# Kernel optimization log

Measured on AMD Instinct MI355X. Metric: run time of the kernel, lower is better.

The kernel has to match this reference:

```python
import jax, jax.numpy as jnp
import numpy as np
from jax import lax

D2 = 712  # 2*(CHAR_EMBED_DIM+ELMO_EMBED_DIM)


def _char_cnn(chars, char_emb, conv_w, conv_b):
    # chars [T,L] int -> [T,100]; batched version of the per-token conv loop
    x = char_emb[chars]                      # [T,L,100]
    x = jnp.transpose(x, (0, 2, 1))          # [T,100,L]
    y = lax.conv_general_dilated(x, conv_w, (1,), [(2, 2)],
                                 dimension_numbers=('NCH', 'OIH', 'NCH'))
    y = y + conv_b[None, :, None]
    return y.max(axis=2)


def _highway(x, pw, pb, gw, gb):
    for i in range(2):
        g = jax.nn.sigmoid(x @ gw[i].T + gb[i])
        p = jax.nn.relu(x @ pw[i].T + pb[i])
        x = g * p + (1.0 - g) * x
    return x


def _lstm_scan(x, Wih, Whh, b, h0, c0):
    # x [T,in]; torch gate order i,f,g,o
    xW = x @ Wih.T + b                       # [T,4H]
    def step(carry, xt):
        h, c = carry
        z = xt + h @ Whh.T
        i, f, g, o = jnp.split(z, 4, axis=-1)
        c = jax.nn.sigmoid(f) * c + jax.nn.sigmoid(i) * jnp.tanh(g)
        h = jax.nn.sigmoid(o) * jnp.tanh(c)
        return (h, c), h
    _, hs = lax.scan(step, (h0, c0), xW)
    return hs


def _bilstm(x, Wih, Whh, b, h0):
    # h0 [2,H]; original uses same tensor for h0 and c0
    f = _lstm_scan(x, Wih[0], Whh[0], b[0], h0[0], h0[0])
    bk = _lstm_scan(x[::-1], Wih[1], Whh[1], b[1], h0[1], h0[1])[::-1]
    return jnp.concatenate([f, bk], axis=-1)


def _forward(chars_ctx, chars_qry, elmo_ctx, elmo_qry, char_emb, conv_w, conv_b,
             hw_plain_w, hw_plain_b, hw_gate_w, hw_gate_b,
             ctx_Wih, ctx_Whh, ctx_b, sim_w,
             mod1_Wih, mod1_Whh, mod1_b, mod2_Wih, mod2_Whh, mod2_b,
             pos_Wih, pos_Whh, pos_b, pos1_w, pos2_w,
             h0_ctx_c, h0_ctx_q, h0_mod, h0_pos):
    def embed(chars, elmo, h0):
        cnn = _char_cnn(chars, char_emb, conv_w, conv_b)
        x = jnp.concatenate([cnn, elmo], axis=1)           # [T,356]
        x = _highway(x, hw_plain_w, hw_plain_b, hw_gate_w, hw_gate_b)
        return _bilstm(x, ctx_Wih, ctx_Whh, ctx_b, h0)     # [T,712]

    C = embed(chars_ctx, elmo_ctx, h0_ctx_c)   # [Tc,712]
    Q = embed(chars_qry, elmo_qry, h0_ctx_q)   # [Tq,712]

    # similarity alpha([c;q;c*q]) decomposed (no bias -> exact same math)
    w_c, w_q, w_cq = sim_w[:D2], sim_w[D2:2 * D2], sim_w[2 * D2:]
    sim = (C @ w_c)[:, None] + (Q @ w_q)[None, :] + (C * w_cq) @ Q.T  # [Tc,Tq]

    c2q = jax.nn.softmax(sim, axis=1) @ Q                  # [Tc,712]
    q2c = jax.nn.softmax(sim.max(axis=1), axis=0) @ C      # [712]
    qac = jnp.concatenate([C, c2q, C * c2q, C * q2c[None, :]], axis=1)  # [Tc,2848]

    M = _bilstm(qac, mod1_Wih, mod1_Whh, mod1_b, h0_mod[0:2])
    M = _bilstm(M, mod2_Wih, mod2_Whh, mod2_b, h0_mod[2:4])  # [Tc,712]

    pos1 = jax.nn.softmax(jnp.concatenate([qac, M], axis=1) @ pos1_w, axis=0)

    M2 = _bilstm(M, pos_Wih, pos_Whh, pos_b, h0_pos)        # [Tc,712]
    pos2 = jax.nn.softmax(jnp.concatenate([qac, M2], axis=1) @ pos2_w, axis=0)
    return pos1, pos2


def setup_inputs() -> dict:
    key = jax.random.key(0)
    ks = jax.random.split(key, 32)
    s = 0.05
    d = {
        'chars_ctx': jax.random.randint(ks[0], (4096, 16), 0, 96, dtype=jnp.int32),
        'chars_qry': jax.random.randint(ks[1], (128, 16), 0, 96, dtype=jnp.int32),
        'elmo_ctx': jax.random.normal(ks[2], (4096, 256), jnp.float32),
        'elmo_qry': jax.random.normal(ks[3], (128, 256), jnp.float32),
        'char_emb': jax.random.normal(ks[4], (96, 100), jnp.float32),
        'conv_w': jax.random.normal(ks[5], (100, 100, 5), jnp.float32) * s,
        'conv_b': jnp.zeros((100,), jnp.float32),
        'hw_plain_w': jax.random.normal(ks[6], (2, 356, 356), jnp.float32) * s,
        'hw_plain_b': jnp.zeros((2, 356), jnp.float32),
        'hw_gate_w': jax.random.normal(ks[7], (2, 356, 356), jnp.float32) * s,
        'hw_gate_b': jnp.zeros((2, 356), jnp.float32),
        'ctx_Wih': jax.random.normal(ks[8], (2, 1424, 356), jnp.float32) * s,
        'ctx_Whh': jax.random.normal(ks[9], (2, 1424, 356), jnp.float32) * s,
        'ctx_b': jnp.zeros((2, 1424), jnp.float32),
        'sim_w': jax.random.normal(ks[10], (2136,), jnp.float32) * s,
        'mod1_Wih': jax.random.normal(ks[11], (2, 1424, 2848), jnp.float32) * s,
        'mod1_Whh': jax.random.normal(ks[12], (2, 1424, 356), jnp.float32) * s,
        'mod1_b': jnp.zeros((2, 1424), jnp.float32),
        'mod2_Wih': jax.random.normal(ks[13], (2, 1424, 712), jnp.float32) * s,
        'mod2_Whh': jax.random.normal(ks[14], (2, 1424, 356), jnp.float32) * s,
        'mod2_b': jnp.zeros((2, 1424), jnp.float32),
        'pos_Wih': jax.random.normal(ks[15], (2, 1424, 712), jnp.float32) * s,
        'pos_Whh': jax.random.normal(ks[16], (2, 1424, 356), jnp.float32) * s,
        'pos_b': jnp.zeros((2, 1424), jnp.float32),
        'pos1_w': jax.random.normal(ks[17], (3560,), jnp.float32) * s,
        'pos2_w': jax.random.normal(ks[18], (3560,), jnp.float32) * s,
        'h0_ctx_c': jax.random.normal(ks[19], (2, 356), jnp.float32) * 0.1,
        'h0_ctx_q': jax.random.normal(ks[20], (2, 356), jnp.float32) * 0.1,
        'h0_mod': jax.random.normal(ks[21], (4, 356), jnp.float32) * 0.1,
        'h0_pos': jax.random.normal(ks[22], (2, 356), jnp.float32) * 0.1,
    }
    return d


def reference(chars_ctx, chars_qry, elmo_ctx, elmo_qry, char_emb, conv_w, conv_b,
              hw_plain_w, hw_plain_b, hw_gate_w, hw_gate_b,
              ctx_Wih, ctx_Whh, ctx_b, sim_w,
              mod1_Wih, mod1_Whh, mod1_b, mod2_Wih, mod2_Whh, mod2_b,
              pos_Wih, pos_Whh, pos_b, pos1_w, pos2_w,
              h0_ctx_c, h0_ctx_q, h0_mod, h0_pos):
    return _forward(chars_ctx, chars_qry, elmo_ctx, elmo_qry, char_emb, conv_w, conv_b,
                    hw_plain_w, hw_plain_b, hw_gate_w, hw_gate_b,
                    ctx_Wih, ctx_Whh, ctx_b, sim_w,
                    mod1_Wih, mod1_Whh, mod1_b, mod2_Wih, mod2_Whh, mod2_b,
                    pos_Wih, pos_Whh, pos_b, pos1_w, pos2_w,
                    h0_ctx_c, h0_ctx_q, h0_mod, h0_pos)
```

## Files before the change

### kernel.cpp

```cpp
#include <hip/hip_runtime.h>
#include <math.h>

__device__ __forceinline__ float sigm(float x) { return 1.0f / (1.0f + __expf(-x)); }

__device__ __forceinline__ float waveSum(float v) {
#pragma unroll
  for (int off = 32; off > 0; off >>= 1) v += __shfl_xor(v, off);
  return v;
}

__global__ __launch_bounds__(128) void cnn_embed_kernel(
    const int* __restrict__ chars_ctx, const int* __restrict__ chars_qry,
    const float* __restrict__ elmo_ctx, const float* __restrict__ elmo_qry,
    const float* __restrict__ char_emb, const float* __restrict__ conv_w,
    const float* __restrict__ conv_b, float* __restrict__ x_all)
{
  int n = blockIdx.x;
  const int*   chars = (n < 4096) ? (chars_ctx + n * 16) : (chars_qry + (n - 4096) * 16);
  const float* elmo  = (n < 4096) ? (elmo_ctx + (size_t)n * 256)
                                  : (elmo_qry + (size_t)(n - 4096) * 256);
  __shared__ float xl[1600];
  __shared__ int   cidx[16];
  int tid = threadIdx.x;
  if (tid < 16) cidx[tid] = chars[tid];
  __syncthreads();
  for (int e = tid; e < 1600; e += 128) {
    int i = e >> 4, p = e & 15;
    xl[e] = char_emb[cidx[p] * 100 + i];
  }
  __syncthreads();
  if (tid < 100) {
    int o = tid;
    float acc[16];
#pragma unroll
    for (int p = 0; p < 16; ++p) acc[p] = 0.f;
    const float* wo = conv_w + o * 500;
    for (int i = 0; i < 100; ++i) {
      const float* xi = xl + i * 16;
#pragma unroll
      for (int k = 0; k < 5; ++k) {
        float w = wo[i * 5 + k];
#pragma unroll
        for (int p = 0; p < 16; ++p) {
          int src = p + k - 2;
          if (src >= 0 && src < 16) acc[p] += w * xi[src];
        }
      }
    }
    float m = acc[0];
#pragma unroll
    for (int p = 1; p < 16; ++p) m = fmaxf(m, acc[p]);
    x_all[(size_t)n * 356 + o] = m + conv_b[o];
  }
  for (int j = tid; j < 256; j += 128)
    x_all[(size_t)n * 356 + 100 + j] = elmo[j];
}

#define GBM 128
#define GBN 128
#define GBK 16

__global__ __launch_bounds__(256) void gemm_abt(
    const float* __restrict__ A, const float* __restrict__ B,
    const float* __restrict__ bias, float* __restrict__ C,
    int M, int N, int K)
{
  __shared__ float As[GBK][GBM + 4];
  __shared__ float Bs[GBK][GBN + 4];
  int tid = threadIdx.x;
  int bm = blockIdx.y * GBM, bn = blockIdx.x * GBN;
  int tx = tid & 15, ty = tid >> 4;
  float acc[8][8];
#pragma unroll
  for (int i = 0; i < 8; ++i)
#pragma unroll
    for (int j = 0; j < 8; ++j) acc[i][j] = 0.f;

  for (int k0 = 0; k0 < K; k0 += GBK) {
    bool fullk = (k0 + GBK <= K);
#pragma unroll
    for (int l = 0; l < 2; ++l) {
      int slot = tid * 2 + l;
      int r = slot >> 2, kq = slot & 3;
      int gm = bm + r, gk = k0 + kq * 4;
      float vx = 0.f, vy = 0.f, vz = 0.f, vw = 0.f;
      if (gm < M) {
        if (fullk) {
          float4 v = *reinterpret_cast<const float4*>(&A[(size_t)gm * K + gk]);
          vx = v.x; vy = v.y; vz = v.z; vw = v.w;
        } else {
          const float* ar = A + (size_t)gm * K;
          if (gk + 0 < K) vx = ar[gk + 0];
          if (gk + 1 < K) vy = ar[gk + 1];
          if (gk + 2 < K) vz = ar[gk + 2];
          if (gk + 3 < K) vw = ar[gk + 3];
        }
      }
      As[kq * 4 + 0][r] = vx;
      As[kq * 4 + 1][r] = vy;
      As[kq * 4 + 2][r] = vz;
      As[kq * 4 + 3][r] = vw;
    }
#pragma unroll
    for (int l = 0; l < 2; ++l) {
      int slot = tid * 2 + l;
      int r = slot >> 2, kq = slot & 3;
      int gn = bn + r, gk = k0 + kq * 4;
      float vx = 0.f, vy = 0.f, vz = 0.f, vw = 0.f;
      if (gn < N) {
        if (fullk) {
          float4 v = *reinterpret_cast<const float4*>(&B[(size_t)gn * K + gk]);
          vx = v.x; vy = v.y; vz = v.z; vw = v.w;
        } else {
          const float* br = B + (size_t)gn * K;
          if (gk + 0 < K) vx = br[gk + 0];
          if (gk + 1 < K) vy = br[gk + 1];
          if (gk + 2 < K) vz = br[gk + 2];
          if (gk + 3 < K) vw = br[gk + 3];
        }
      }
      Bs[kq * 4 + 0][r] = vx;
      Bs[kq * 4 + 1][r] = vy;
      Bs[kq * 4 + 2][r] = vz;
      Bs[kq * 4 + 3][r] = vw;
    }
    __syncthreads();
#pragma unroll
    for (int kk = 0; kk < GBK; ++kk) {
      float a[8], b[8];
#pragma unroll
      for (int i = 0; i < 8; ++i) a[i] = As[kk][ty + 16 * i];
#pragma unroll
      for (int j = 0; j < 8; ++j) b[j] = Bs[kk][tx + 16 * j];
#pragma unroll
      for (int i = 0; i < 8; ++i)
#pragma unroll
        for (int j = 0; j < 8; ++j) acc[i][j] += a[i] * b[j];
    }
    __syncthreads();
  }

  float bv[8];
#pragma unroll
  for (int j = 0; j < 8; ++j) {
    int gn = bn + tx + 16 * j;
    bv[j] = (bias && gn < N) ? bias[gn] : 0.f;
  }
#pragma unroll
  for (int i = 0; i < 8; ++i) {
    int gm = bm + ty + 16 * i;
    if (gm >= M) continue;
    float* crow = C + (size_t)gm * N;
#pragma unroll
    for (int j = 0; j < 8; ++j) {
      int gn = bn + tx + 16 * j;
      if (gn < N) crow[gn] = acc[i][j] + bv[j];
    }
  }
}

__global__ void highway_combine(float* __restrict__ x, const float* __restrict__ g,
                                const float* __restrict__ p, int total)
{
  int i = blockIdx.x * blockDim.x + threadIdx.x;
  if (i < total) {
    float gg = sigm(g[i]);
    float pp = fmaxf(p[i], 0.f);
    x[i] = gg * pp + (1.f - gg) * x[i];
  }
}

#define NWG 16
#define SLICE 23

__global__ __launch_bounds__(512, 1) void lstm_scan_kernel(
    const float* __restrict__ xw, const float* __restrict__ whh,
    const float* __restrict__ h0, float* __restrict__ out,
    int row0, int N, unsigned long long* exbuf,
    const float* __restrict__ h0b, int row0b, int Nb,
    unsigned long long* exbufb)
{
  int bid = blockIdx.x;
  if (bid >= 2 * NWG) {
    bid -= 2 * NWG;
    h0 = h0b; row0 = row0b; N = Nb; exbuf = exbufb;
    if (N <= 0) return;
  }
  const int tid  = threadIdx.x;
  const int dir  = bid & 1;
  const int wg   = bid >> 1;
  const int lane = tid & 63;
  const int wv   = tid >> 6;
  const int li   = lane & 15;
  const int g16  = lane >> 4;
  const int j0   = wg * SLICE;
  const float* whh_d = whh + (size_t)dir * 1424 * 356;
  const float* h0_d  = h0 + dir * 356;
  const int xcol0 = dir * 1424;
  const int ocol0 = dir * 356;
  unsigned long long* exd = exbuf + (size_t)dir * 712;

  __shared__ float h_lds[384];
  __shared__ float z_lds[4 * SLICE];

  float wreg[3][24];
#pragma unroll
  for (int b = 0; b < 3; ++b) {
    int rr = wv * 12 + g16 * 3 + b;
    bool rv = (rr < 4 * SLICE);
    int gate = rv ? (rr / SLICE) : 0, jj = rv ? (rr % SLICE) : 0;
    int j = j0 + jj;
    bool v = rv && (j < 356);
    const float* wrow = whh_d + (size_t)(gate * 356 + j) * 356;
#pragma unroll
    for (int m = 0; m < 24; ++m) {
      int k = li + 16 * m;
      wreg[b][m] = (v && m < 23 && k < 356) ? wrow[k] : 0.f;
    }
  }

  for (int k = tid; k < 384; k += 512) {
    int a = k / 24, m = k % 24;
    int j = a + 16 * m;
    h_lds[k] = (m < 23 && j < 356) ? h0_d[j] : 0.f;
  }

  const bool guown = (tid < SLICE) && (j0 + tid) < 356;
  const int  jg    = j0 + (guown ? tid : 0);
  float c_reg = guown ? h0_d[jg] : 0.f;

  float xw_cur[4];
  {
    int row = dir ? (N - 1) : 0;
    size_t rb = (size_t)(row0 + row) * 2848;
#pragma unroll
    for (int g = 0; g < 4; ++g)
      xw_cur[g] = guown ? xw[rb + (size_t)(xcol0 + g * 356 + jg)] : 0.f;
  }
  __syncthreads();

  for (int t = 0; t < N; ++t) {
    int row = dir ? (N - 1 - t) : t;
    size_t grow = (size_t)(row0 + row);

    float xw_nx[4];
#pragma unroll
    for (int g = 0; g < 4; ++g) xw_nx[g] = 0.f;
    if (t + 1 < N) {
      int rown = dir ? (N - 2 - t) : (t + 1);
      size_t rb = (size_t)(row0 + rown) * 2848;
#pragma unroll
      for (int g = 0; g < 4; ++g)
        xw_nx[g] = guown ? xw[rb + (size_t)(xcol0 + g * 356 + jg)] : 0.f;
    }

    float hh[24];
#pragma unroll
    for (int q4 = 0; q4 < 6; ++q4) {
      float4 hv = *reinterpret_cast<const float4*>(&h_lds[li * 24 + q4 * 4]);
      hh[q4 * 4 + 0] = hv.x; hh[q4 * 4 + 1] = hv.y;
      hh[q4 * 4 + 2] = hv.z; hh[q4 * 4 + 3] = hv.w;
    }

    float s[3];
#pragma unroll
    for (int b = 0; b < 3; ++b) {
      float v = wreg[b][0] * hh[0];
#pragma unroll
      for (int m = 1; m < 24; ++m) v += wreg[b][m] * hh[m];
      s[b] = v;
    }
#pragma unroll
    for (int off = 8; off > 0; off >>= 1) {
#pragma unroll
      for (int b = 0; b < 3; ++b) s[b] += __shfl_xor(s[b], off);
    }
    if (li == 0) {
#pragma unroll
      for (int b = 0; b < 3; ++b) {
        int rr = wv * 12 + g16 * 3 + b;
        if (rr < 4 * SLICE) z_lds[rr] = s[b];
      }
    }
    __syncthreads();

    if (guown) {
      float zi = z_lds[tid]             + xw_cur[0];
      float zf = z_lds[SLICE + tid]     + xw_cur[1];
      float zg = z_lds[2 * SLICE + tid] + xw_cur[2];
      float zo = z_lds[3 * SLICE + tid] + xw_cur[3];
      float c = sigm(zf) * c_reg + sigm(zi) * tanhf(zg);
      float h = sigm(zo) * tanhf(c);
      c_reg = c;
      unsigned long long pk =
          ((unsigned long long)(unsigned)(t + 1) << 32) |
          (unsigned long long)__float_as_uint(h);
      __hip_atomic_store(&exd[(size_t)(t & 1) * 356 + jg], pk,
                         __ATOMIC_RELAXED, __HIP_MEMORY_SCOPE_AGENT);
      out[grow * 712 + ocol0 + jg] = h;
    }
    if (t + 1 < N && tid < 356) {
      unsigned long long* p = &exd[(size_t)(t & 1) * 356 + tid];
      unsigned ep = (unsigned)(t + 1);
      unsigned long long v;
      do {
        v = __hip_atomic_load(p, __ATOMIC_RELAXED, __HIP_MEMORY_SCOPE_AGENT);
      } while ((unsigned)(v >> 32) != ep);
      h_lds[(tid & 15) * 24 + (tid >> 4)] = __uint_as_float((unsigned)v);
    }
    __syncthreads();

#pragma unroll
    for (int g = 0; g < 4; ++g) xw_cur[g] = xw_nx[g];
  }
}

__global__ __launch_bounds__(64) void qdot_kernel(
    const float* __restrict__ Q, const float* __restrict__ sim_w, float* __restrict__ s2)
{
  int j = blockIdx.x;
  int lane = threadIdx.x;
  const float* q  = Q + (size_t)j * 712;
  const float* wq = sim_w + 712;
  float s = 0.f;
  for (int k = lane; k < 712; k += 64) s += q[k] * wq[k];
  s = waveSum(s);
  if (lane == 0) s2[j] = s;
}

__global__ __launch_bounds__(256) void attn_row_kernel(
    const float* __restrict__ CQ, const float* __restrict__ sim_w,
    const float* __restrict__ s2, float* __restrict__ rowm, float* __restrict__ qac)
{
  int i = blockIdx.x;
  int tid = threadIdx.x;
  const float* Q = CQ + (size_t)4096 * 712;
  __shared__ float crow[712], cw[712], prow[128], red[256];
  const float* ci = CQ + (size_t)i * 712;

  float s1p = 0.f;
  for (int k = tid; k < 712; k += 256) {
    float v = ci[k];
    crow[k] = v;
    cw[k] = v * sim_w[1424 + k];
    s1p += v * sim_w[k];
  }
  red[tid] = s1p;
  __syncthreads();
  for (int s = 128; s > 0; s >>= 1) { if (tid < s) red[tid] += red[tid + s]; __syncthreads(); }
  float s1 = red[0];

  int lane = tid & 63, wv = tid >> 6;
  for (int j = wv; j < 128; j += 4) {
    const float* qj = Q + (size_t)j * 712;
    float s = 0.f;
    for (int k = lane; k < 712; k += 64) s += cw[k] * qj[k];
    s = waveSum(s);
    if (lane == 0) prow[j] = s1 + s2[j] + s;
  }
  __syncthreads();

  float v = (tid < 128) ? prow[tid] : -1e30f;
  red[tid] = v;
  __syncthreads();
  for (int s = 128; s > 0; s >>= 1) { if (tid < s) red[tid] = fmaxf(red[tid], red[tid + s]); __syncthreads(); }
  float m = red[0];
  __syncthreads();
  float e = (tid < 128) ? __expf(prow[tid] - m) : 0.f;
  red[tid] = e;
  __syncthreads();
  for (int s = 128; s > 0; s >>= 1) { if (tid < s) red[tid] += red[tid + s]; __syncthreads(); }
  float denom = red[0];
  if (tid < 128) prow[tid] = e / denom;
  if (tid == 0) rowm[i] = m;
  __syncthreads();

  size_t qb = (size_t)i * 2848;
  for (int k = tid; k < 712; k += 256) {
    float acc = 0.f;
    for (int j = 0; j < 128; ++j) acc += prow[j] * Q[(size_t)j * 712 + k];
    float cv = crow[k];
    qac[qb + k]        = cv;
    qac[qb + 712 + k]  = acc;
    qac[qb + 1424 + k] = cv * acc;
  }
}

__global__ __launch_bounds__(256) void softmax_4096(const float* __restrict__ in,
                                                    float* __restrict__ out)
{
  __shared__ float red[256];
  int tid = threadIdx.x;
  float m = -1e30f;
  for (int i = tid; i < 4096; i += 256) m = fmaxf(m, in[i]);
  red[tid] = m;
  __syncthreads();
  for (int s = 128; s > 0; s >>= 1) { if (tid < s) red[tid] = fmaxf(red[tid], red[tid + s]); __syncthreads(); }
  m = red[0];
  __syncthreads();
  float sum = 0.f;
  for (int i = tid; i < 4096; i += 256) sum += __expf(in[i] - m);
  red[tid] = sum;
  __syncthreads();
  for (int s = 128; s > 0; s >>= 1) { if (tid < s) red[tid] += red[tid + s]; __syncthreads(); }
  float denom = red[0];
  for (int i = tid; i < 4096; i += 256) out[i] = __expf(in[i] - m) / denom;
}

__global__ __launch_bounds__(256) void q2c_kernel(
    const float* __restrict__ CQ, const float* __restrict__ rowa, float* __restrict__ q2c)
{
  int k = blockIdx.x * 256 + threadIdx.x;
  if (k < 712) {
    float acc = 0.f;
    for (int i = 0; i < 4096; ++i) acc += rowa[i] * CQ[(size_t)i * 712 + k];
    q2c[k] = acc;
  }
}

__global__ __launch_bounds__(256) void qac_finish_kernel(
    const float* __restrict__ CQ, const float* __restrict__ q2c, float* __restrict__ qac)
{
  int i = blockIdx.x;
  int tid = threadIdx.x;
  for (int k = tid; k < 712; k += 256)
    qac[(size_t)i * 2848 + 2136 + k] = CQ[(size_t)i * 712 + k] * q2c[k];
}

__global__ __launch_bounds__(256) void logits_kernel(
    const float* __restrict__ qac, const float* __restrict__ Mx,
    const float* __restrict__ w, float* __restrict__ logits)
{
  int i = blockIdx.x, tid = threadIdx.x;
  __shared__ float red[256];
  float s = 0.f;
  const float* qr = qac + (size_t)i * 2848;
  for (int k = tid; k < 2848; k += 256) s += qr[k] * w[k];
  const float* mr = Mx + (size_t)i * 712;
  for (int k = tid; k < 712; k += 256) s += mr[k] * w[2848 + k];
  red[tid] = s;
  __syncthreads();
  for (int st = 128; st > 0; st >>= 1) { if (tid < st) red[tid] += red[tid + st]; __syncthreads(); }
  if (tid == 0) logits[i] = red[0];
}

extern "C" void kernel_launch(void* const* d_in, const int* in_sizes, int n_in,
                              void* d_out, int out_size, void* d_ws, size_t ws_size,
                              hipStream_t stream)
{
  const int*   chars_ctx = (const int*)d_in[0];
  const int*   chars_qry = (const int*)d_in[1];
  const float* elmo_ctx  = (const float*)d_in[2];
  const float* elmo_qry  = (const float*)d_in[3];
  const float* char_emb  = (const float*)d_in[4];
  const float* conv_w    = (const float*)d_in[5];
  const float* conv_b    = (const float*)d_in[6];
  const float* hw_plain_w = (const float*)d_in[7];
  const float* hw_plain_b = (const float*)d_in[8];
  const float* hw_gate_w  = (const float*)d_in[9];
  const float* hw_gate_b  = (const float*)d_in[10];
  const float* ctx_Wih   = (const float*)d_in[11];
  const float* ctx_Whh   = (const float*)d_in[12];
  const float* ctx_b     = (const float*)d_in[13];
  const float* sim_w     = (const float*)d_in[14];
  const float* mod1_Wih  = (const float*)d_in[15];
  const float* mod1_Whh  = (const float*)d_in[16];
  const float* mod1_b    = (const float*)d_in[17];
  const float* mod2_Wih  = (const float*)d_in[18];
  const float* mod2_Whh  = (const float*)d_in[19];
  const float* mod2_b    = (const float*)d_in[20];
  const float* pos_Wih   = (const float*)d_in[21];
  const float* pos_Whh   = (const float*)d_in[22];
  const float* pos_b     = (const float*)d_in[23];
  const float* pos1_w    = (const float*)d_in[24];
  const float* pos2_w    = (const float*)d_in[25];
  const float* h0_ctx_c  = (const float*)d_in[26];
  const float* h0_ctx_q  = (const float*)d_in[27];
  const float* h0_mod    = (const float*)d_in[28];
  const float* h0_pos    = (const float*)d_in[29];
  float* outp = (float*)d_out;

  float* ws = (float*)d_ws;
  size_t off = 0;
  auto alloc = [&](size_t n) { float* p = ws + off; off += n; return p; };
  float* x_all  = alloc(4224ull * 356);
  float* gbuf   = alloc(4224ull * 356);
  float* pbuf   = alloc(4224ull * 356);
  float* xw_all = alloc(4224ull * 2848);
  float* CQ     = alloc(4224ull * 712);
  float* M1     = alloc(4096ull * 712);
  float* Mm     = alloc(4096ull * 712);
  float* M2     = alloc(4096ull * 712);
  float* qac    = alloc(4096ull * 2848);
  float* s2v    = alloc(128);
  float* rowm   = alloc(4096);
  float* rowa   = alloc(4096);
  float* q2cv   = alloc(1024);
  float* logits = alloc(8192);
  off = (off + 1) & ~(size_t)1;
  unsigned long long* exbuf = (unsigned long long*)(ws + off);
  off += 5ull * 1424 * 2;

  auto cdiv = [](int a, int b) { return (a + b - 1) / b; };

  cnn_embed_kernel<<<4224, 128, 0, stream>>>(chars_ctx, chars_qry, elmo_ctx, elmo_qry,
                                             char_emb, conv_w, conv_b, x_all);

  for (int l = 0; l < 2; ++l) {
    gemm_abt<<<dim3(cdiv(356, GBN), cdiv(4224, GBM)), 256, 0, stream>>>(
        x_all, hw_gate_w + (size_t)l * 356 * 356, hw_gate_b + l * 356, gbuf, 4224, 356, 356);
    gemm_abt<<<dim3(cdiv(356, GBN), cdiv(4224, GBM)), 256, 0, stream>>>(
        x_all, hw_plain_w + (size_t)l * 356 * 356, hw_plain_b + l * 356, pbuf, 4224, 356, 356);
    highway_combine<<<cdiv(4224 * 356, 256), 256, 0, stream>>>(x_all, gbuf, pbuf, 4224 * 356);
  }

  gemm_abt<<<dim3(cdiv(2848, GBN), cdiv(4224, GBM)), 256, 0, stream>>>(
      x_all, ctx_Wih, ctx_b, xw_all, 4224, 2848, 356);
  lstm_scan_kernel<<<4 * NWG, 512, 0, stream>>>(xw_all, ctx_Whh, h0_ctx_c, CQ, 0, 4096,
                                                exbuf + 0ull * 1424,
                                                h0_ctx_q, 4096, 128,
                                                exbuf + 1ull * 1424);

  qdot_kernel<<<128, 64, 0, stream>>>(CQ + 4096ull * 712, sim_w, s2v);
  attn_row_kernel<<<4096, 256, 0, stream>>>(CQ, sim_w, s2v, rowm, qac);
  softmax_4096<<<1, 256, 0, stream>>>(rowm, rowa);
  q2c_kernel<<<cdiv(712, 256), 256, 0, stream>>>(CQ, rowa, q2cv);
  qac_finish_kernel<<<4096, 256, 0, stream>>>(CQ, q2cv, qac);

  gemm_abt<<<dim3(cdiv(2848, GBN), cdiv(4096, GBM)), 256, 0, stream>>>(
      qac, mod1_Wih, mod1_b, xw_all, 4096, 2848, 2848);
  lstm_scan_kernel<<<2 * NWG, 512, 0, stream>>>(xw_all, mod1_Whh, h0_mod, M1, 0, 4096,
                                                exbuf + 2ull * 1424,
                                                nullptr, 0, 0, nullptr);

  gemm_abt<<<dim3(cdiv(2848, GBN), cdiv(4096, GBM)), 256, 0, stream>>>(
      M1, mod2_Wih, mod2_b, xw_all, 4096, 2848, 712);
  lstm_scan_kernel<<<2 * NWG, 512, 0, stream>>>(xw_all, mod2_Whh, h0_mod + 712, Mm, 0, 4096,
                                                exbuf + 3ull * 1424,
                                                nullptr, 0, 0, nullptr);

  logits_kernel<<<4096, 256, 0, stream>>>(qac, Mm, pos1_w, logits);
  softmax_4096<<<1, 256, 0, stream>>>(logits, outp);

  gemm_abt<<<dim3(cdiv(2848, GBN), cdiv(4096, GBM)), 256, 0, stream>>>(
      Mm, pos_Wih, pos_b, xw_all, 4096, 2848, 712);
  lstm_scan_kernel<<<2 * NWG, 512, 0, stream>>>(xw_all, pos_Whh, h0_pos, M2, 0, 4096,
                                                exbuf + 4ull * 1424,
                                                nullptr, 0, 0, nullptr);
  logits_kernel<<<4096, 256, 0, stream>>>(qac, M2, pos2_w, logits + 4096);
  softmax_4096<<<1, 256, 0, stream>>>(logits + 4096, outp + 4096);

  (void)in_sizes; (void)n_in; (void)out_size; (void)ws_size;
}
```

Measured before the change: 34.90 ms.

## Assign all four gates per hidden unit to one lane group, removing mid-step barrier

Remaps the persistent LSTM recurrence kernel so each 16-lane group computes all four gate dot products for one hidden unit, instead of spreading gate rows across groups and exchanging them through shared memory. This removes the intermediate z_lds exchange and one __syncthreads per timestep. h and the xW inputs are now double-buffered in LDS, with padded stride 28, so a single barrier per step is enough. The per-step critical path gets shorter, at the cost of more registers per thread (4x24 weights) and fewer threads doing the gate math.

```diff
diff --git a/kernel.cpp b/kernel.cpp
--- a/kernel.cpp
+++ b/kernel.cpp
@@ -192,7 +192,7 @@
   const int lane = tid & 63;
   const int wv   = tid >> 6;
   const int li   = lane & 15;
-  const int g16  = lane >> 4;
+  const int grp  = wv * 4 + (lane >> 4);
   const int j0   = wg * SLICE;
   const float* whh_d = whh + (size_t)dir * 1424 * 356;
   const float* h0_d  = h0 + dir * 356;
@@ -200,118 +200,109 @@
   const int ocol0 = dir * 356;
   unsigned long long* exd = exbuf + (size_t)dir * 712;
 
-  __shared__ float h_lds[384];
-  __shared__ float z_lds[4 * SLICE];
-
-  float wreg[3][24];
-#pragma unroll
-  for (int b = 0; b < 3; ++b) {
-    int rr = wv * 12 + g16 * 3 + b;
-    bool rv = (rr < 4 * SLICE);
-    int gate = rv ? (rr / SLICE) : 0, jj = rv ? (rr % SLICE) : 0;
-    int j = j0 + jj;
-    bool v = rv && (j < 356);
-    const float* wrow = whh_d + (size_t)(gate * 356 + j) * 356;
+  __shared__ float h_lds[2][448];
+  __shared__ float xw_lds[2][92];
+
+  const bool gown = (grp < SLICE) && (j0 + grp) < 356;
+  const int  ju   = j0 + (gown ? grp : 0);
+
+  float wreg[4][24];
+#pragma unroll
+  for (int g = 0; g < 4; ++g) {
+    const float* wrow = whh_d + (size_t)(g * 356 + ju) * 356;
 #pragma unroll
     for (int m = 0; m < 24; ++m) {
       int k = li + 16 * m;
-      wreg[b][m] = (v && m < 23 && k < 356) ? wrow[k] : 0.f;
-    }
-  }
-
-  for (int k = tid; k < 384; k += 512) {
-    int a = k / 24, m = k % 24;
+      wreg[g][m] = (gown && m < 23 && k < 356) ? wrow[k] : 0.f;
+    }
+  }
+
+  for (int k = tid; k < 448; k += 512) {
+    int a = k / 28, m = k % 28;
     int j = a + 16 * m;
-    h_lds[k] = (m < 23 && j < 356) ? h0_d[j] : 0.f;
-  }
-
-  const bool guown = (tid < SLICE) && (j0 + tid) < 356;
-  const int  jg    = j0 + (guown ? tid : 0);
-  float c_reg = guown ? h0_d[jg] : 0.f;
-
-  float xw_cur[4];
-  {
+    h_lds[0][k] = (m < 23 && j < 356) ? h0_d[j] : 0.f;
+    h_lds[1][k] = 0.f;
+  }
+
+  float c_reg = (gown && li == 0) ? h0_d[ju] : 0.f;
+
+  const int  xgate = tid / 23, xjj = tid % 23;
+  const bool xduty = (tid < 92) && (j0 + xjj) < 356;
+  const size_t xcol = (size_t)(xcol0 + xgate * 356 + (j0 + xjj));
+
+  if (tid < 92) {
     int row = dir ? (N - 1) : 0;
-    size_t rb = (size_t)(row0 + row) * 2848;
-#pragma unroll
-    for (int g = 0; g < 4; ++g)
-      xw_cur[g] = guown ? xw[rb + (size_t)(xcol0 + g * 356 + jg)] : 0.f;
+    xw_lds[0][tid] = xduty ? xw[(size_t)(row0 + row) * 2848 + xcol] : 0.f;
   }
   __syncthreads();
 
   for (int t = 0; t < N; ++t) {
     int row = dir ? (N - 1 - t) : t;
     size_t grow = (size_t)(row0 + row);
-
-    float xw_nx[4];
-#pragma unroll
-    for (int g = 0; g < 4; ++g) xw_nx[g] = 0.f;
-    if (t + 1 < N) {
+    const int par = t & 1;
+
+    float xw_nx = 0.f;
+    if (t + 1 < N && xduty) {
       int rown = dir ? (N - 2 - t) : (t + 1);
-      size_t rb = (size_t)(row0 + rown) * 2848;
-#pragma unroll
-      for (int g = 0; g < 4; ++g)
-        xw_nx[g] = guown ? xw[rb + (size_t)(xcol0 + g * 356 + jg)] : 0.f;
-    }
-
-    float hh[24];
-#pragma unroll
-    for (int q4 = 0; q4 < 6; ++q4) {
-      float4 hv = *reinterpret_cast<const float4*>(&h_lds[li * 24 + q4 * 4]);
-      hh[q4 * 4 + 0] = hv.x; hh[q4 * 4 + 1] = hv.y;
-      hh[q4 * 4 + 2] = hv.z; hh[q4 * 4 + 3] = hv.w;
-    }
-
-    float s[3];
-#pragma unroll
-    for (int b = 0; b < 3; ++b) {
-      float v = wreg[b][0] * hh[0];
-#pragma unroll
-      for (int m = 1; m < 24; ++m) v += wreg[b][m] * hh[m];
-      s[b] = v;
-    }
-#pragma unroll
-    for (int off = 8; off > 0; off >>= 1) {
-#pragma unroll
-      for (int b = 0; b < 3; ++b) s[b] += __shfl_xor(s[b], off);
-    }
-    if (li == 0) {
-#pragma unroll
-      for (int b = 0; b < 3; ++b) {
-        int rr = wv * 12 + g16 * 3 + b;
-        if (rr < 4 * SLICE) z_lds[rr] = s[b];
-      }
-    }
-    __syncthreads();
-
-    if (guown) {
-      float zi = z_lds[tid]             + xw_cur[0];
-      float zf = z_lds[SLICE + tid]     + xw_cur[1];
-      float zg = z_lds[2 * SLICE + tid] + xw_cur[2];
-      float zo = z_lds[3 * SLICE + tid] + xw_cur[3];
+      xw_nx = xw[(size_t)(row0 + rown) * 2848 + xcol];
+    }
+
+    float s0 = 0.f, s1 = 0.f, s2 = 0.f, s3 = 0.f;
+    if (grp < SLICE) {
+      float hh[24];
+#pragma unroll
+      for (int q4 = 0; q4 < 6; ++q4) {
+        float4 hv = *reinterpret_cast<const float4*>(&h_lds[par][li * 28 + q4 * 4]);
+        hh[q4 * 4 + 0] = hv.x; hh[q4 * 4 + 1] = hv.y;
+        hh[q4 * 4 + 2] = hv.z; hh[q4 * 4 + 3] = hv.w;
+      }
+#pragma unroll
+      for (int m = 0; m < 24; ++m) {
+        float h = hh[m];
+        s0 += wreg[0][m] * h;
+        s1 += wreg[1][m] * h;
+        s2 += wreg[2][m] * h;
+        s3 += wreg[3][m] * h;
+      }
+#pragma unroll
+      for (int off = 8; off > 0; off >>= 1) {
+        s0 += __shfl_xor(s0, off);
+        s1 += __shfl_xor(s1, off);
+        s2 += __shfl_xor(s2, off);
+        s3 += __shfl_xor(s3, off);
+      }
+    }
+
+    if (gown && li == 0) {
+      float zi = s0 + xw_lds[par][grp];
+      float zf = s1 + xw_lds[par][23 + grp];
+      float zg = s2 + xw_lds[par][46 + grp];
+      float zo = s3 + xw_lds[par][69 + grp];
       float c = sigm(zf) * c_reg + sigm(zi) * tanhf(zg);
       float h = sigm(zo) * tanhf(c);
       c_reg = c;
       unsigned long long pk =
           ((unsigned long long)(unsigned)(t + 1) << 32) |
           (unsigned long long)__float_as_uint(h);
-      __hip_atomic_store(&exd[(size_t)(t & 1) * 356 + jg], pk,
+      __hip_atomic_store(&exd[(size_t)par * 356 + ju], pk,
                          __ATOMIC_RELAXED, __HIP_MEMORY_SCOPE_AGENT);
-      out[grow * 712 + ocol0 + jg] = h;
-    }
-    if (t + 1 < N && tid < 356) {
-      unsigned long long* p = &exd[(size_t)(t & 1) * 356 + tid];
-      unsigned ep = (unsigned)(t + 1);
-      unsigned long long v;
-      do {
-        v = __hip_atomic_load(p, __ATOMIC_RELAXED, __HIP_MEMORY_SCOPE_AGENT);
-      } while ((unsigned)(v >> 32) != ep);
-      h_lds[(tid & 15) * 24 + (tid >> 4)] = __uint_as_float((unsigned)v);
+      out[grow * 712 + ocol0 + ju] = h;
+    }
+
+    if (t + 1 < N) {
+      if (tid < 92) xw_lds[par ^ 1][tid] = xw_nx;
+      if (tid < 356) {
+        unsigned long long* p = &exd[(size_t)par * 356 + tid];
+        unsigned ep = (unsigned)(t + 1);
+        unsigned long long v;
+        do {
+          v = __hip_atomic_load(p, __ATOMIC_RELAXED, __HIP_MEMORY_SCOPE_AGENT);
+        } while ((unsigned)(v >> 32) != ep);
+        h_lds[par ^ 1][(tid & 15) * 28 + (tid >> 4)] =
+            __uint_as_float((unsigned)v);
+      }
     }
     __syncthreads();
-
-#pragma unroll
-    for (int g = 0; g < 4; ++g) xw_cur[g] = xw_nx[g];
   }
 }
 
```

Result: slower. 37.05 ms (+6.2%).
